# Performance work log

Hardware: AMD Instinct MI355X
Metric: run time of the kernel (lower is better)

## Reference

```python
import jax, jax.numpy as jnp
import numpy as np
import math

N_NODES = 100_000
N_EDGES = 800_000
NODE_DIM = 128
EDGE_DIM = 64
HIDDEN = 128
HEADS = 8
HEAD_DIM = HIDDEN // HEADS


def _segment_softmax(scores, seg, n):
    # scores: [E, H], grouped by destination node `seg`
    m = jax.ops.segment_max(scores, seg, num_segments=n)
    e = jnp.exp(scores - m[seg])
    d = jax.ops.segment_sum(e, seg, num_segments=n)
    return e / d[seg]


def _layer_norm(x, g, b, eps=1e-5):
    mu = jnp.mean(x, axis=-1, keepdims=True)
    var = jnp.mean((x - mu) ** 2, axis=-1, keepdims=True)
    return (x - mu) * jax.lax.rsqrt(var + eps) * g + b


def _graph_conv(x, row, col, edge_proj, Wn, b, n):
    # PyG GraphConvolution: add self-loops, symmetric deg normalization,
    # msg = (Wn x)[row] + edge_lin(edge_attr); aggregate (add) at col.
    # Self-loop edges carry zero edge features (edge_lin has no bias -> contributes 0).
    loop = jnp.arange(n)
    row2 = jnp.concatenate([row, loop])
    col2 = jnp.concatenate([col, loop])
    ep2 = jnp.concatenate([edge_proj, jnp.zeros((n, edge_proj.shape[1]), edge_proj.dtype)])
    deg = jax.ops.segment_sum(jnp.ones_like(col2, x.dtype), col2, num_segments=n)
    dinv = jnp.where(deg > 0, jax.lax.rsqrt(jnp.maximum(deg, 1e-12)), 0.0)
    norm = dinv[row2] * dinv[col2]
    h = x @ Wn                                   # [n, hidden]
    msg = (h[row2] + ep2) * norm[:, None]        # [E+n, hidden]
    return jax.ops.segment_sum(msg, col2, num_segments=n) + b


def setup_inputs() -> dict:
    key = jax.random.key(0)
    ks = jax.random.split(key, 20)

    def xav(k, shape):
        fan_in, fan_out = shape[0], shape[-1]
        s = math.sqrt(2.0 / (fan_in + fan_out))
        return jax.random.normal(k, shape, jnp.float32) * s

    return {
        "x": jax.random.normal(ks[0], (N_NODES, NODE_DIM), jnp.float32),
        "edge_index": jax.random.randint(ks[1], (2, N_EDGES), 0, N_NODES, jnp.int64),
        "edge_attr": jax.random.normal(ks[2], (N_EDGES, EDGE_DIM), jnp.float32),
        "W_qkv": xav(ks[3], (NODE_DIM, 3 * HIDDEN)),
        "b_qkv": jnp.zeros((3 * HIDDEN,), jnp.float32),
        "W_ek": xav(ks[4], (EDGE_DIM, HIDDEN)),
        "b_ek": jnp.zeros((HIDDEN,), jnp.float32),
        "W_n1": xav(ks[5], (NODE_DIM, HIDDEN)),
        "W_e1": xav(ks[6], (EDGE_DIM, HIDDEN)),
        "b1": jnp.zeros((HIDDEN,), jnp.float32),
        "W_n2": xav(ks[7], (HIDDEN, HIDDEN)),
        "W_e2": xav(ks[8], (EDGE_DIM, HIDDEN)),
        "b2": jnp.zeros((HIDDEN,), jnp.float32),
        "W_out": xav(ks[9], (HIDDEN, NODE_DIM)),
        "b_out": jnp.zeros((NODE_DIM,), jnp.float32),
        "ln_g": jnp.ones((NODE_DIM,), jnp.float32),
        "ln_b": jnp.zeros((NODE_DIM,), jnp.float32),
    }


def reference(x, edge_index, edge_attr, W_qkv, b_qkv, W_ek, b_ek,
              W_n1, W_e1, b1, W_n2, W_e2, b2, W_out, b_out, ln_g, ln_b):
    n = x.shape[0]
    row, col = edge_index[0], edge_index[1]

    # --- compute_dynamic_edges (computed in the original forward but its
    # result is discarded; kept here for fidelity to the source math) ---
    qkv = x @ W_qkv + b_qkv
    q, k, _v = jnp.split(qkv, 3, axis=-1)
    q = q.reshape(n, HEADS, HEAD_DIM)
    k = k.reshape(n, HEADS, HEAD_DIM)
    ek = (edge_attr @ W_ek + b_ek).reshape(-1, HEADS, HEAD_DIM)
    scores = jnp.sum(q[row] * (k[col] + ek), axis=-1) / math.sqrt(HEAD_DIM)  # [E, H]
    _edge_weights = _segment_softmax(scores, col, n)  # unused downstream (as in source)

    # --- two GraphConvolution layers (dropout is identity in eval mode) ---
    h1 = jax.nn.gelu(_graph_conv(x, row, col, edge_attr @ W_e1, W_n1, b1, n), approximate=False)
    h2 = jax.nn.gelu(_graph_conv(h1, row, col, edge_attr @ W_e2, W_n2, b2, n), approximate=False)

    out = h2 @ W_out + b_out
    return _layer_norm(out + x, ln_g, ln_b)
```

## Files before the change

### kernel.cpp

```cpp
#include <hip/hip_runtime.h>
#include <math.h>

#define N_NODES 100000
#define N_EDGES 800000
#define NBLK 391

__global__ void k_count(const int* __restrict__ col, int* __restrict__ cnt) {
    int e = blockIdx.x * 256 + threadIdx.x;
    if (e < N_EDGES) {
        unsigned c = (unsigned)col[e];
        if (c < N_NODES) atomicAdd(&cnt[c], 1);
    }
}

__global__ void k_blocksum(const int* __restrict__ cnt, int* __restrict__ bsum) {
    __shared__ int sc[256];
    int t = threadIdx.x, i = blockIdx.x * 256 + t;
    sc[t] = (i < N_NODES) ? cnt[i] : 0;
    __syncthreads();
    for (int o = 128; o; o >>= 1) {
        if (t < o) sc[t] += sc[t + o];
        __syncthreads();
    }
    if (t == 0) bsum[blockIdx.x] = sc[0];
}

__global__ void k_scanblocks(const int* __restrict__ bsum, int* __restrict__ bexcl) {
    __shared__ int s[512];
    int t = threadIdx.x;
    s[t] = (t < NBLK) ? bsum[t] : 0;
    __syncthreads();
    for (int o = 1; o < 512; o <<= 1) {
        int v = (t >= o) ? s[t - o] : 0;
        __syncthreads();
        s[t] += v;
        __syncthreads();
    }
    if (t < NBLK) bexcl[t] = t ? s[t - 1] : 0;
}

__global__ void k_offsets(const int* __restrict__ cnt, const int* __restrict__ bexcl,
                          int* __restrict__ off, int* __restrict__ pos,
                          int2* __restrict__ offcnt) {
    __shared__ int sc[256];
    int t = threadIdx.x, i = blockIdx.x * 256 + t;
    int v = (i < N_NODES) ? cnt[i] : 0;
    sc[t] = v;
    __syncthreads();
    for (int o = 1; o < 256; o <<= 1) {
        int tv = (t >= o) ? sc[t - o] : 0;
        __syncthreads();
        sc[t] += tv;
        __syncthreads();
    }
    if (i < N_NODES) {
        int s = bexcl[blockIdx.x] + (sc[t] - v);
        off[i] = s;
        pos[i] = s;
        if (offcnt) offcnt[i] = make_int2(s, v);
    }
}

__global__ void k_dinv(const int* __restrict__ cnt, float* __restrict__ dinv) {
    int i = blockIdx.x * 256 + threadIdx.x;
    if (i < N_NODES) dinv[i] = rsqrtf((float)(cnt[i] + 1));
}

__global__ void k_build(const int* __restrict__ row, const int* __restrict__ col,
                        int* __restrict__ pos, const float* __restrict__ dinv,
                        int* __restrict__ srcE, int* __restrict__ eidE,
                        float* __restrict__ dinvE) {
    int e = blockIdx.x * 256 + threadIdx.x;
    if (e < N_EDGES) {
        unsigned r = (unsigned)row[e], c = (unsigned)col[e];
        if (r < N_NODES && c < N_NODES) {
            int slot = atomicAdd(&pos[c], 1);
            srcE[slot] = (int)r;
            eidE[slot] = e;
            if (dinvE) dinvE[slot] = dinv[r];
        }
    }
}

template<int MODE>
__global__ __launch_bounds__(256) void k_gather(
    const float* __restrict__ X, const float* __restrict__ EAraw,
    const int2* __restrict__ offcnt,
    const int* __restrict__ srcE, const int* __restrict__ eidE,
    const float* __restrict__ dinvE, const float* __restrict__ dinv,
    float* __restrict__ act)
{
    int w = threadIdx.x >> 6, l = threadIdx.x & 63;
    int c = blockIdx.x * 4 + w;
    if (c >= N_NODES) return;
    int2 oc = offcnt[c];
    int beg = __builtin_amdgcn_readfirstlane(oc.x);
    int d   = __builtin_amdgcn_readfirstlane(oc.y);
    const float2* X2 = (const float2*)X;

    float2 xc = X2[(size_t)c * 64 + l];
    float dv = dinv[c];

    int sU[16]; float vU[16]; int eU[16];
    #pragma unroll
    for (int i = 0; i < 16; i++) sU[i] = srcE[beg + i];
    #pragma unroll
    for (int i = 0; i < 16; i++) vU[i] = dinvE[beg + i];
    if (MODE == 0) {
        #pragma unroll
        for (int i = 0; i < 16; i++) eU[i] = eidE[beg + i];
    }
    int s0 = (d > 0) ? sU[0] : 0;
    int e0 = (d > 0) ? eU[0] : 0;
    #pragma unroll
    for (int i = 0; i < 16; i++) {
        if (i >= d) {
            vU[i] = 0.f;
            sU[i] = s0;
            if (MODE == 0) eU[i] = e0;
        }
    }

    float2 xv[16];
    #pragma unroll
    for (int i = 0; i < 16; i++) xv[i] = X2[(size_t)sU[i] * 64 + l];
    float evv[16];
    if (MODE == 0) {
        #pragma unroll
        for (int i = 0; i < 16; i++) evv[i] = EAraw[(size_t)eU[i] * 64 + l];
    }

    float a0 = 0.f, a1 = 0.f, ae = 0.f;
    #pragma unroll
    for (int i = 0; i < 16; i++) {
        a0 += vU[i] * xv[i].x;
        a1 += vU[i] * xv[i].y;
        if (MODE == 0) ae += vU[i] * evv[i];
    }

    for (int j = 16; j < d; j++) {
        int s = srcE[beg + j];
        float v = dinvE[beg + j];
        float2 x = X2[(size_t)s * 64 + l];
        a0 += v * x.x;
        a1 += v * x.y;
        if (MODE == 0) ae += v * EAraw[(size_t)eidE[beg + j] * 64 + l];
    }

    float dv2 = dv * dv;
    float* arow = act + (size_t)c * 192;
    ((float2*)arow)[l] = make_float2(dv * a0 + dv2 * xc.x, dv * a1 + dv2 * xc.y);
    if (MODE == 0) arow[128 + l] = dv * ae;
}

__global__ __launch_bounds__(256, 3) void k_gemm(
    const float* __restrict__ act,
    const float* __restrict__ Wn, const float* __restrict__ We,
    const float* __restrict__ bias, float* __restrict__ out)
{
    __shared__ float sact[64][192];
    int t = threadIdx.x;
    int w = t >> 6, l = t & 63;

    const size_t CAP = (size_t)N_NODES * 192;
    size_t base = (size_t)blockIdx.x * (64 * 192);
    #pragma unroll
    for (int i = 0; i < 12; i++) {
        size_t fi = base + (size_t)(i * 256 + t) * 4;
        float4 v = make_float4(0.f, 0.f, 0.f, 0.f);
        if (fi + 4 <= CAP) v = *(const float4*)(act + fi);
        *(float4*)&sact[0][(i * 256 + t) * 4] = v;
    }
    __syncthreads();

    int row0 = blockIdx.x * 64 + w * 16;
    float acc[16][2] = {};

    const float2* Wn2 = (const float2*)Wn;
    for (int k = 0; k < 128; k += 4) {
        float2 w0 = Wn2[(k + 0) * 64 + l];
        float2 w1 = Wn2[(k + 1) * 64 + l];
        float2 w2 = Wn2[(k + 2) * 64 + l];
        float2 w3 = Wn2[(k + 3) * 64 + l];
        #pragma unroll
        for (int r = 0; r < 16; r++) {
            float4 a = *(const float4*)&sact[w * 16 + r][k];
            acc[r][0] += a.x * w0.x + a.y * w1.x + a.z * w2.x + a.w * w3.x;
            acc[r][1] += a.x * w0.y + a.y * w1.y + a.z * w2.y + a.w * w3.y;
        }
    }

    const float2* We2 = (const float2*)We;
    for (int k = 0; k < 64; k += 4) {
        float2 w0 = We2[(k + 0) * 64 + l];
        float2 w1 = We2[(k + 1) * 64 + l];
        float2 w2 = We2[(k + 2) * 64 + l];
        float2 w3 = We2[(k + 3) * 64 + l];
        #pragma unroll
        for (int r = 0; r < 16; r++) {
            float4 a = *(const float4*)&sact[w * 16 + r][128 + k];
            acc[r][0] += a.x * w0.x + a.y * w1.x + a.z * w2.x + a.w * w3.x;
            acc[r][1] += a.x * w0.y + a.y * w1.y + a.z * w2.y + a.w * w3.y;
        }
    }

    float2 bb = ((const float2*)bias)[l];
    #pragma unroll
    for (int r = 0; r < 16; r++) {
        int c = row0 + r;
        if (c >= N_NODES) break;
        float v0 = acc[r][0] + bb.x;
        float v1 = acc[r][1] + bb.y;
        v0 = 0.5f * v0 * (1.0f + erff(v0 * 0.70710678f));
        v1 = 0.5f * v1 * (1.0f + erff(v1 * 0.70710678f));
        ((float2*)out)[(size_t)c * 64 + l] = make_float2(v0, v1);
    }
}

__global__ __launch_bounds__(256) void k_layer(
    const float* __restrict__ X, const float* __restrict__ EAraw,
    const float* __restrict__ EaIn, float* __restrict__ EaOut,
    const int* __restrict__ off, const int* __restrict__ cnt,
    const int* __restrict__ srcE, const int* __restrict__ eidE,
    const float* __restrict__ dinv,
    const float* __restrict__ Wn, const float* __restrict__ We,
    const float* __restrict__ bias, float* __restrict__ out, int mode)
{
    __shared__ float act[4][4][192];
    int w = threadIdx.x >> 6, l = threadIdx.x & 63;
    int row0 = blockIdx.x * 16 + w * 4;

    for (int r = 0; r < 4; r++) {
        int c = row0 + r;
        int beg = off[c];
        int d = cnt[c];
        float a0 = 0.f, a1 = 0.f, ae = 0.f;
        for (int j = 0; j < d; j++) {
            unsigned s = (unsigned)srcE[beg + j];
            if (s >= N_NODES) continue;
            float sv = dinv[s];
            float2 xv = ((const float2*)X)[s * 64 + l];
            a0 += sv * xv.x;
            a1 += sv * xv.y;
            if (mode == 0) {
                unsigned e = (unsigned)eidE[beg + j];
                if (e < N_EDGES) ae += sv * EAraw[e * 64 + l];
            }
        }
        float dv = dinv[c], dv2 = dv * dv;
        float2 xc = ((const float2*)X)[c * 64 + l];
        act[w][r][2 * l]     = dv * a0 + dv2 * xc.x;
        act[w][r][2 * l + 1] = dv * a1 + dv2 * xc.y;
        if (mode == 0) {
            act[w][r][128 + l] = dv * ae;
            EaOut[c * 64 + l] = ae;
        } else {
            act[w][r][128 + l] = dv * EaIn[c * 64 + l];
        }
    }
    __syncthreads();

    float acc[4][2] = {};
    for (int k = 0; k < 128; k++) {
        float2 wv = ((const float2*)Wn)[k * 64 + l];
        #pragma unroll
        for (int r = 0; r < 4; r++) {
            float a = act[w][r][k];
            acc[r][0] += a * wv.x;
            acc[r][1] += a * wv.y;
        }
    }
    for (int k = 0; k < 64; k++) {
        float2 wv = ((const float2*)We)[k * 64 + l];
        #pragma unroll
        for (int r = 0; r < 4; r++) {
            float a = act[w][r][128 + k];
            acc[r][0] += a * wv.x;
            acc[r][1] += a * wv.y;
        }
    }

    float2 bb = ((const float2*)bias)[l];
    for (int r = 0; r < 4; r++) {
        float v0 = acc[r][0] + bb.x;
        float v1 = acc[r][1] + bb.y;
        v0 = 0.5f * v0 * (1.0f + erff(v0 * 0.70710678f));
        v1 = 0.5f * v1 * (1.0f + erff(v1 * 0.70710678f));
        ((float2*)out)[(row0 + r) * 64 + l] = make_float2(v0, v1);
    }
}

__global__ __launch_bounds__(256) void k_final(
    const float* __restrict__ h2, const float* __restrict__ x,
    const float* __restrict__ Wo, const float* __restrict__ bo,
    const float* __restrict__ g, const float* __restrict__ lb,
    float* __restrict__ out)
{
    __shared__ float lds[4][4][128];
    int w = threadIdx.x >> 6, l = threadIdx.x & 63;
    int row0 = blockIdx.x * 16 + w * 4;

    for (int r = 0; r < 4; r++) {
        int c = row0 + r;
        float2 hv = ((const float2*)h2)[(size_t)c * 64 + l];
        lds[w][r][2 * l]     = hv.x;
        lds[w][r][2 * l + 1] = hv.y;
    }
    __syncthreads();

    float acc[4][2] = {};
    const float2* Wo2 = (const float2*)Wo;
    for (int k = 0; k < 128; k += 4) {
        float2 w0 = Wo2[(k + 0) * 64 + l];
        float2 w1 = Wo2[(k + 1) * 64 + l];
        float2 w2 = Wo2[(k + 2) * 64 + l];
        float2 w3 = Wo2[(k + 3) * 64 + l];
        #pragma unroll
        for (int r = 0; r < 4; r++) {
            float4 a = *(const float4*)&lds[w][r][k];
            acc[r][0] += a.x * w0.x + a.y * w1.x + a.z * w2.x + a.w * w3.x;
            acc[r][1] += a.x * w0.y + a.y * w1.y + a.z * w2.y + a.w * w3.y;
        }
    }

    float2 bov = ((const float2*)bo)[l];
    float2 gv  = ((const float2*)g)[l];
    float2 lbv = ((const float2*)lb)[l];

    for (int r = 0; r < 4; r++) {
        int c = row0 + r;
        float2 xv = ((const float2*)x)[(size_t)c * 64 + l];
        float v0 = acc[r][0] + bov.x + xv.x;
        float v1 = acc[r][1] + bov.y + xv.y;
        float s = v0 + v1;
        #pragma unroll
        for (int o = 32; o; o >>= 1) s += __shfl_xor(s, o, 64);
        float mu = s * (1.0f / 128.0f);
        float d0 = v0 - mu, d1 = v1 - mu;
        float sq = d0 * d0 + d1 * d1;
        #pragma unroll
        for (int o = 32; o; o >>= 1) sq += __shfl_xor(sq, o, 64);
        float rs = rsqrtf(sq * (1.0f / 128.0f) + 1e-5f);
        float2 ov;
        ov.x = d0 * rs * gv.x + lbv.x;
        ov.y = d1 * rs * gv.y + lbv.y;
        ((float2*)out)[(size_t)c * 64 + l] = ov;
    }
}

extern "C" void kernel_launch(void* const* d_in, const int* in_sizes, int n_in,
                              void* d_out, int out_size, void* d_ws, size_t ws_size,
                              hipStream_t stream)
{
    const float* x   = (const float*)d_in[0];
    const int*   ei  = (const int*)d_in[1];
    const float* ea  = (const float*)d_in[2];
    const float* Wn1 = (const float*)d_in[7];
    const float* We1 = (const float*)d_in[8];
    const float* b1  = (const float*)d_in[9];
    const float* Wn2 = (const float*)d_in[10];
    const float* We2 = (const float*)d_in[11];
    const float* b2  = (const float*)d_in[12];
    const float* Wo  = (const float*)d_in[13];
    const float* bo  = (const float*)d_in[14];
    const float* lng = (const float*)d_in[15];
    const float* lnb = (const float*)d_in[16];
    const int* row = ei;
    const int* col = ei + N_EDGES;

    char* ws = (char*)d_ws;
    size_t off_b = 0;
    auto alloc = [&](size_t bytes) {
        void* p = ws + off_b;
        off_b += (bytes + 255) & ~(size_t)255;
        return p;
    };
    int*   cnt   = (int*)  alloc((size_t)N_NODES * 4);
    int*   off   = (int*)  alloc((size_t)N_NODES * 4);
    int*   pos   = (int*)  alloc((size_t)N_NODES * 4);
    int*   bsum  = (int*)  alloc((size_t)NBLK * 4);
    int*   bexcl = (int*)  alloc((size_t)NBLK * 4);
    float* dinv  = (float*)alloc((size_t)N_NODES * 4);
    int*   srcE  = (int*)  alloc((size_t)(N_EDGES + 16) * 4);
    int*   eidE  = (int*)  alloc((size_t)(N_EDGES + 16) * 4);
    float* h1    = (float*)alloc((size_t)N_NODES * 128 * 4);
    size_t common_end = off_b;

    float* dinvE  = (float*)alloc((size_t)(N_EDGES + 16) * 4);
    int2*  offcnt = (int2*) alloc((size_t)N_NODES * 8);
    float* act    = (float*)alloc((size_t)N_NODES * 192 * 4);
    size_t split_end = off_b;

    float* Ea = (float*)(ws + common_end);
    size_t fused_end = common_end + (((size_t)N_NODES * 64 * 4 + 255) & ~(size_t)255);

    bool use_split = (split_end <= ws_size);
    if (!use_split && fused_end > ws_size) return;

    float* h2 = (float*)d_out;

    hipMemsetAsync(cnt, 0, (size_t)N_NODES * 4, stream);

    k_count     <<<(N_EDGES + 255) / 256, 256, 0, stream>>>(col, cnt);
    k_blocksum  <<<NBLK, 256, 0, stream>>>(cnt, bsum);
    k_scanblocks<<<1, 512, 0, stream>>>(bsum, bexcl);
    k_offsets   <<<NBLK, 256, 0, stream>>>(cnt, bexcl, off, pos,
                                           use_split ? offcnt : nullptr);
    k_dinv      <<<NBLK, 256, 0, stream>>>(cnt, dinv);
    k_build     <<<(N_EDGES + 255) / 256, 256, 0, stream>>>(
        row, col, pos, dinv, srcE, eidE, use_split ? dinvE : nullptr);

    if (use_split) {
        k_gather<0><<<(N_NODES + 3) / 4, 256, 0, stream>>>(x, ea, offcnt,
                                                           srcE, eidE, dinvE, dinv, act);
        k_gemm  <<<(N_NODES + 63) / 64, 256, 0, stream>>>(act, Wn1, We1, b1, h1);
        k_gather<1><<<(N_NODES + 3) / 4, 256, 0, stream>>>(h1, nullptr, offcnt,
                                                           srcE, eidE, dinvE, dinv, act);
        k_gemm  <<<(N_NODES + 63) / 64, 256, 0, stream>>>(act, Wn2, We2, b2, h2);
    } else {
        k_layer<<<N_NODES / 16, 256, 0, stream>>>(x, ea, nullptr, Ea,
                                                  off, cnt, srcE, eidE, dinv,
                                                  Wn1, We1, b1, h1, 0);
        k_layer<<<N_NODES / 16, 256, 0, stream>>>(h1, nullptr, Ea, nullptr,
                                                  off, cnt, srcE, eidE, dinv,
                                                  Wn2, We2, b2, h2, 1);
    }
    k_final<<<N_NODES / 16, 256, 0, stream>>>(h2, x, Wo, bo, lng, lnb, (float*)d_out);
}
```

Before: 879.6 us.

## Pack CSR edge arrays into int4 and fuse final projection into second GEMM

Merges the separate source, edge-id and source-dinv arrays into one int4 record per CSR slot, so each edge needs a single vector load in the gather kernels. Folds the dinv computation into the offsets kernel, removing one launch. Fuses the output projection, residual add and layer norm into the second-layer GEMM, so h2 is never written to or reread from global memory. The cost is a wider edge record: 16 bytes per edge instead of 8 or 12, with one padding word.

```diff
diff --git a/kernel.cpp b/kernel.cpp
--- a/kernel.cpp
+++ b/kernel.cpp
@@ -41,7 +41,7 @@
 
 __global__ void k_offsets(const int* __restrict__ cnt, const int* __restrict__ bexcl,
                           int* __restrict__ off, int* __restrict__ pos,
-                          int2* __restrict__ offcnt) {
+                          int2* __restrict__ offcnt, float* __restrict__ dinv) {
     __shared__ int sc[256];
     int t = threadIdx.x, i = blockIdx.x * 256 + t;
     int v = (i < N_NODES) ? cnt[i] : 0;
@@ -58,26 +58,19 @@
         off[i] = s;
         pos[i] = s;
         if (offcnt) offcnt[i] = make_int2(s, v);
-    }
-}
-
-__global__ void k_dinv(const int* __restrict__ cnt, float* __restrict__ dinv) {
-    int i = blockIdx.x * 256 + threadIdx.x;
-    if (i < N_NODES) dinv[i] = rsqrtf((float)(cnt[i] + 1));
+        dinv[i] = rsqrtf((float)(v + 1));
+    }
 }
 
 __global__ void k_build(const int* __restrict__ row, const int* __restrict__ col,
                         int* __restrict__ pos, const float* __restrict__ dinv,
-                        int* __restrict__ srcE, int* __restrict__ eidE,
-                        float* __restrict__ dinvE) {
+                        int4* __restrict__ edge) {
     int e = blockIdx.x * 256 + threadIdx.x;
     if (e < N_EDGES) {
         unsigned r = (unsigned)row[e], c = (unsigned)col[e];
         if (r < N_NODES && c < N_NODES) {
             int slot = atomicAdd(&pos[c], 1);
-            srcE[slot] = (int)r;
-            eidE[slot] = e;
-            if (dinvE) dinvE[slot] = dinv[r];
+            edge[slot] = make_int4((int)r, e, __float_as_int(dinv[r]), 0);
         }
     }
 }
@@ -85,10 +78,8 @@
 template<int MODE>
 __global__ __launch_bounds__(256) void k_gather(
     const float* __restrict__ X, const float* __restrict__ EAraw,
-    const int2* __restrict__ offcnt,
-    const int* __restrict__ srcE, const int* __restrict__ eidE,
-    const float* __restrict__ dinvE, const float* __restrict__ dinv,
-    float* __restrict__ act)
+    const int2* __restrict__ offcnt, const int4* __restrict__ edge,
+    const float* __restrict__ dinv, float* __restrict__ act)
 {
     int w = threadIdx.x >> 6, l = threadIdx.x & 63;
     int c = blockIdx.x * 4 + w;
@@ -103,12 +94,11 @@
 
     int sU[16]; float vU[16]; int eU[16];
     #pragma unroll
-    for (int i = 0; i < 16; i++) sU[i] = srcE[beg + i];
-    #pragma unroll
-    for (int i = 0; i < 16; i++) vU[i] = dinvE[beg + i];
-    if (MODE == 0) {
-        #pragma unroll
-        for (int i = 0; i < 16; i++) eU[i] = eidE[beg + i];
+    for (int i = 0; i < 16; i++) {
+        int4 E = edge[beg + i];
+        sU[i] = E.x;
+        eU[i] = E.y;
+        vU[i] = __int_as_float(E.z);
     }
     int s0 = (d > 0) ? sU[0] : 0;
     int e0 = (d > 0) ? eU[0] : 0;
@@ -117,7 +107,7 @@
         if (i >= d) {
             vU[i] = 0.f;
             sU[i] = s0;
-            if (MODE == 0) eU[i] = e0;
+            eU[i] = e0;
         }
     }
 
@@ -139,12 +129,12 @@
     }
 
     for (int j = 16; j < d; j++) {
-        int s = srcE[beg + j];
-        float v = dinvE[beg + j];
-        float2 x = X2[(size_t)s * 64 + l];
+        int4 E = edge[beg + j];
+        float v = __int_as_float(E.z);
+        float2 x = X2[(size_t)E.x * 64 + l];
         a0 += v * x.x;
         a1 += v * x.y;
-        if (MODE == 0) ae += v * EAraw[(size_t)eidE[beg + j] * 64 + l];
+        if (MODE == 0) ae += v * EAraw[(size_t)E.y * 64 + l];
     }
 
     float dv2 = dv * dv;
@@ -189,7 +179,6 @@
             acc[r][1] += a.x * w0.y + a.y * w1.y + a.z * w2.y + a.w * w3.y;
         }
     }
-
     const float2* We2 = (const float2*)We;
     for (int k = 0; k < 64; k += 4) {
         float2 w0 = We2[(k + 0) * 64 + l];
@@ -217,12 +206,121 @@
     }
 }
 
+__global__ __launch_bounds__(256, 3) void k_gemm_final(
+    const float* __restrict__ act,
+    const float* __restrict__ Wn, const float* __restrict__ We,
+    const float* __restrict__ bias, const float* __restrict__ x,
+    const float* __restrict__ Wo, const float* __restrict__ bo,
+    const float* __restrict__ g, const float* __restrict__ lb,
+    float* __restrict__ out)
+{
+    __shared__ float sact[64][192];
+    int t = threadIdx.x;
+    int w = t >> 6, l = t & 63;
+
+    const size_t CAP = (size_t)N_NODES * 192;
+    size_t base = (size_t)blockIdx.x * (64 * 192);
+    #pragma unroll
+    for (int i = 0; i < 12; i++) {
+        size_t fi = base + (size_t)(i * 256 + t) * 4;
+        float4 v = make_float4(0.f, 0.f, 0.f, 0.f);
+        if (fi + 4 <= CAP) v = *(const float4*)(act + fi);
+        *(float4*)&sact[0][(i * 256 + t) * 4] = v;
+    }
+    __syncthreads();
+
+    int row0 = blockIdx.x * 64 + w * 16;
+    float acc[16][2] = {};
+
+    const float2* Wn2 = (const float2*)Wn;
+    for (int k = 0; k < 128; k += 4) {
+        float2 w0 = Wn2[(k + 0) * 64 + l];
+        float2 w1 = Wn2[(k + 1) * 64 + l];
+        float2 w2 = Wn2[(k + 2) * 64 + l];
+        float2 w3 = Wn2[(k + 3) * 64 + l];
+        #pragma unroll
+        for (int r = 0; r < 16; r++) {
+            float4 a = *(const float4*)&sact[w * 16 + r][k];
+            acc[r][0] += a.x * w0.x + a.y * w1.x + a.z * w2.x + a.w * w3.x;
+            acc[r][1] += a.x * w0.y + a.y * w1.y + a.z * w2.y + a.w * w3.y;
+        }
+    }
+    const float2* We2 = (const float2*)We;
+    for (int k = 0; k < 64; k += 4) {
+        float2 w0 = We2[(k + 0) * 64 + l];
+        float2 w1 = We2[(k + 1) * 64 + l];
+        float2 w2 = We2[(k + 2) * 64 + l];
+        float2 w3 = We2[(k + 3) * 64 + l];
+        #pragma unroll
+        for (int r = 0; r < 16; r++) {
+            float4 a = *(const float4*)&sact[w * 16 + r][128 + k];
+            acc[r][0] += a.x * w0.x + a.y * w1.x + a.z * w2.x + a.w * w3.x;
+            acc[r][1] += a.x * w0.y + a.y * w1.y + a.z * w2.y + a.w * w3.y;
+        }
+    }
+
+    float2 bb = ((const float2*)bias)[l];
+    #pragma unroll
+    for (int r = 0; r < 16; r++) {
+        float v0 = acc[r][0] + bb.x;
+        float v1 = acc[r][1] + bb.y;
+        v0 = 0.5f * v0 * (1.0f + erff(v0 * 0.70710678f));
+        v1 = 0.5f * v1 * (1.0f + erff(v1 * 0.70710678f));
+        sact[w * 16 + r][2 * l]     = v0;
+        sact[w * 16 + r][2 * l + 1] = v1;
+        acc[r][0] = 0.f;
+        acc[r][1] = 0.f;
+    }
+
+    const float2* Wo2 = (const float2*)Wo;
+    for (int k = 0; k < 128; k += 4) {
+        float2 w0 = Wo2[(k + 0) * 64 + l];
+        float2 w1 = Wo2[(k + 1) * 64 + l];
+        float2 w2 = Wo2[(k + 2) * 64 + l];
+        float2 w3 = Wo2[(k + 3) * 64 + l];
+        #pragma unroll
+        for (int r = 0; r < 16; r++) {
+            float4 a = *(const float4*)&sact[w * 16 + r][k];
+            acc[r][0] += a.x * w0.x + a.y * w1.x + a.z * w2.x + a.w * w3.x;
+            acc[r][1] += a.x * w0.y + a.y * w1.y + a.z * w2.y + a.w * w3.y;
+        }
+    }
+
+    float2 bov = ((const float2*)bo)[l];
+    float2 gv  = ((const float2*)g)[l];
+    float2 lbv = ((const float2*)lb)[l];
+    const float2* X2 = (const float2*)x;
+
+    #pragma unroll
+    for (int r = 0; r < 16; r++) {
+        int c = row0 + r;
+        bool ok = (c < N_NODES);
+        float2 xv = ok ? X2[(size_t)c * 64 + l] : make_float2(0.f, 0.f);
+        float v0 = acc[r][0] + bov.x + xv.x;
+        float v1 = acc[r][1] + bov.y + xv.y;
+        float s = v0 + v1;
+        #pragma unroll
+        for (int o = 32; o; o >>= 1) s += __shfl_xor(s, o, 64);
+        float mu = s * (1.0f / 128.0f);
+        float d0 = v0 - mu, d1 = v1 - mu;
+        float sq = d0 * d0 + d1 * d1;
+        #pragma unroll
+        for (int o = 32; o; o >>= 1) sq += __shfl_xor(sq, o, 64);
+        float rs = rsqrtf(sq * (1.0f / 128.0f) + 1e-5f);
+        if (ok) {
+            float2 ov;
+            ov.x = d0 * rs * gv.x + lbv.x;
+            ov.y = d1 * rs * gv.y + lbv.y;
+            ((float2*)out)[(size_t)c * 64 + l] = ov;
+        }
+    }
+}
+
 __global__ __launch_bounds__(256) void k_layer(
     const float* __restrict__ X, const float* __restrict__ EAraw,
     const float* __restrict__ EaIn, float* __restrict__ EaOut,
     const int* __restrict__ off, const int* __restrict__ cnt,
-    const int* __restrict__ srcE, const int* __restrict__ eidE,
-    const float* __restrict__ dinv,
+    const int4* __restrict__ edge, const float* __restrict__ dinv,
     const float* __restrict__ Wn, const float* __restrict__ We,
     const float* __restrict__ bias, float* __restrict__ out, int mode)
 {
@@ -236,14 +334,15 @@
         int d = cnt[c];
         float a0 = 0.f, a1 = 0.f, ae = 0.f;
         for (int j = 0; j < d; j++) {
-            unsigned s = (unsigned)srcE[beg + j];
+            int4 E = edge[beg + j];
+            unsigned s = (unsigned)E.x;
             if (s >= N_NODES) continue;
-            float sv = dinv[s];
+            float sv = __int_as_float(E.z);
             float2 xv = ((const float2*)X)[s * 64 + l];
             a0 += sv * xv.x;
             a1 += sv * xv.y;
             if (mode == 0) {
-                unsigned e = (unsigned)eidE[beg + j];
+                unsigned e = (unsigned)E.y;
                 if (e < N_EDGES) ae += sv * EAraw[e * 64 + l];
             }
         }
@@ -381,12 +480,10 @@
     int*   bsum  = (int*)  alloc((size_t)NBLK * 4);
     int*   bexcl = (int*)  alloc((size_t)NBLK * 4);
     float* dinv  = (float*)alloc((size_t)N_NODES * 4);
-    int*   srcE  = (int*)  alloc((size_t)(N_EDGES + 16) * 4);
-    int*   eidE  = (int*)  alloc((size_t)(N_EDGES + 16) * 4);
+    int4*  edge  = (int4*) alloc((size_t)(N_EDGES + 16) * 16);
     float* h1    = (float*)alloc((size_t)N_NODES * 128 * 4);
     size_t common_end = off_b;
 
-    float* dinvE  = (float*)alloc((size_t)(N_EDGES + 16) * 4);
     int2*  offcnt = (int2*) alloc((size_t)N_NODES * 8);
     float* act    = (float*)alloc((size_t)N_NODES * 192 * 4);
     size_t split_end = off_b;
@@ -405,25 +502,24 @@
     k_blocksum  <<<NBLK, 256, 0, stream>>>(cnt, bsum);
     k_scanblocks<<<1, 512, 0, stream>>>(bsum, bexcl);
     k_offsets   <<<NBLK, 256, 0, stream>>>(cnt, bexcl, off, pos,
-                                           use_split ? offcnt : nullptr);
-    k_dinv      <<<NBLK, 256, 0, stream>>>(cnt, dinv);
-    k_build     <<<(N_EDGES + 255) / 256, 256, 0, stream>>>(
-        row, col, pos, dinv, srcE, eidE, use_split ? dinvE : nullptr);
+                                           use_split ? offcnt : nullptr, dinv);
+    k_build     <<<(N_EDGES + 255) / 256, 256, 0, stream>>>(row, col, pos, dinv, edge);
 
     if (use_split) {
         k_gather<0><<<(N_NODES + 3) / 4, 256, 0, stream>>>(x, ea, offcnt,
-                                                           srcE, eidE, dinvE, dinv, act);
-        k_gemm  <<<(N_NODES + 63) / 64, 256, 0, stream>>>(act, Wn1, We1, b1, h1);
+                                                           edge, dinv, act);
+        k_gemm     <<<(N_NODES + 63) / 64, 256, 0, stream>>>(act, Wn1, We1, b1, h1);
         k_gather<1><<<(N_NODES + 3) / 4, 256, 0, stream>>>(h1, nullptr, offcnt,
-                                                           srcE, eidE, dinvE, dinv, act);
-        k_gemm  <<<(N_NODES + 63) / 64, 256, 0, stream>>>(act, Wn2, We2, b2, h2);
+                                                           edge, dinv, act);
+        k_gemm_final<<<(N_NODES + 63) / 64, 256, 0, stream>>>(
+            act, Wn2, We2, b2, x, Wo, bo, lng, lnb, (float*)d_out);
     } else {
         k_layer<<<N_NODES / 16, 256, 0, stream>>>(x, ea, nullptr, Ea,
-                                                  off, cnt, srcE, eidE, dinv,
+                                                  off, cnt, edge, dinv,
                                                   Wn1, We1, b1, h1, 0);
         k_layer<<<N_NODES / 16, 256, 0, stream>>>(h1, nullptr, Ea, nullptr,
-                                                  off, cnt, srcE, eidE, dinv,
+                                                  off, cnt, edge, dinv,
                                                   Wn2, We2, b2, h2, 1);
-    }
-    k_final<<<N_NODES / 16, 256, 0, stream>>>(h2, x, Wo, bo, lng, lnb, (float*)d_out);
-}
+        k_final<<<N_NODES / 16, 256, 0, stream>>>(h2, x, Wo, bo, lng, lnb, (float*)d_out);
+    }
+}
```

Measured after the change: 853.4 us. -3.0%, faster.
